# Performance work log

Hardware: AMD Instinct MI355X
Metric: run time of the kernel (lower is better)

The kernel has to match this reference:

```python
import jax, jax.numpy as jnp
import numpy as np

LAMBDA_CHAMFER = 1.0
LAMBDA_EDGE = 0.1


def setup_inputs() -> dict:
    key = jax.random.key(0)
    k1, k2, k3 = jax.random.split(key, 3)
    B, N, M, E = 8, 4096, 4096, 12288
    pred_vertices = jax.random.normal(k1, (B, N, 3), dtype=jnp.float32)
    gt_vertices = jax.random.normal(k2, (B, M, 3), dtype=jnp.float32)
    edges = jax.random.randint(k3, (E, 2), 0, N, dtype=jnp.int64)
    return {"pred_vertices": pred_vertices, "gt_vertices": gt_vertices, "edges": edges}


def _pairwise_dist(p1, p2):
    # ||x - y|| computed via the expanded form to avoid a [B,N,M,3] intermediate.
    # dist2[b,n,m] = |p1[b,n]|^2 + |p2[b,m]|^2 - 2 * p1[b,n] . p2[b,m]
    sq1 = jnp.sum(p1 * p1, axis=-1)  # [B, N]
    sq2 = jnp.sum(p2 * p2, axis=-1)  # [B, M]
    cross = jnp.einsum('bnd,bmd->bnm', p1, p2)  # [B, N, M]
    dist2 = sq1[:, :, None] + sq2[:, None, :] - 2.0 * cross
    return jnp.sqrt(jnp.maximum(dist2, 0.0))


def chamfer_distance(p1, p2):
    dist = _pairwise_dist(p1, p2)  # [B, N, M]
    min_p1 = jnp.min(dist, axis=2)  # [B, N] nearest gt for each pred point
    min_p2 = jnp.min(dist, axis=1)  # [B, M] nearest pred for each gt point
    return jnp.mean(min_p1) + jnp.mean(min_p2)


def edge_length_regularization(vertices, edges):
    v1 = vertices[:, edges[:, 0]]  # [B, E, 3]
    v2 = vertices[:, edges[:, 1]]  # [B, E, 3]
    lengths = jnp.linalg.norm(v1 - v2, axis=2)  # [B, E]
    return jnp.var(lengths, ddof=1)  # torch.var is unbiased by default


def reference(pred_vertices, gt_vertices, edges):
    cd = chamfer_distance(pred_vertices, gt_vertices)
    edge_loss = edge_length_regularization(pred_vertices, edges)
    return LAMBDA_CHAMFER * cd + LAMBDA_EDGE * edge_loss
```

## Files before the change

kernel.cpp:

```cpp
#include <hip/hip_runtime.h>
#include <hip/hip_bf16.h>
#include <float.h>

constexpr int B = 8, N = 4096, M = 4096, E = 12288;
constexpr int CBLOCK = 1024;
constexpr int CHAM_BLOCKS = 256;
constexpr int EDGE_BLOCKS = (B * E) / CBLOCK;
constexpr int SPLIT = 8;
constexpr int RPT = M / SPLIT;
constexpr int VEC = 2;
constexpr int QG = CBLOCK / SPLIT;


__global__ __launch_bounds__(CBLOCK) void fused_kernel(
    const float* __restrict__ pred, const float* __restrict__ gt,
    const int* __restrict__ edges, float* __restrict__ ws) {
    const int bid = blockIdx.x;
    const int t = threadIdx.x;

    __shared__ float4 tile[M];
    __shared__ float red[SPLIT * 256];
    __shared__ float wsum[16];

    if (bid < CHAM_BLOCKS) {
        const int dir = bid >> 7;
        const int b   = (bid >> 4) & 7;
        const int qt  = bid & 15;
        const float* __restrict__ q   = dir ? gt   : pred;
        const float* __restrict__ ref = dir ? pred : gt;

        {
            const float2* rb = (const float2*)(ref + (size_t)b * M * 3) + 6 * t;
            const float2 r0 = rb[0], r1 = rb[1], r2 = rb[2];
            const float2 r3 = rb[3], r4 = rb[4], r5 = rb[5];
            const float x0=r0.x,y0=r0.y,z0=r1.x, x1=r1.y,y1=r2.x,z1=r2.y;
            const float x2=r3.x,y2=r3.y,z2=r4.x, x3=r4.y,y3=r5.x,z3=r5.y;
            tile[4*t+0] = make_float4(x0,y0,z0, 0.5f*(x0*x0+y0*y0+z0*z0));
            tile[4*t+1] = make_float4(x1,y1,z1, 0.5f*(x1*x1+y1*y1+z1*z1));
            tile[4*t+2] = make_float4(x2,y2,z2, 0.5f*(x2*x2+y2*y2+z2*z2));
            tile[4*t+3] = make_float4(x3,y3,z3, 0.5f*(x3*x3+y3*y3+z3*z3));
        }

        const int qloc = t & (QG - 1);
        const int s    = t >> 7;
        float qx[VEC], qy[VEC], qz[VEC], h1[VEC];
#pragma unroll
        for (int i = 0; i < VEC; i++) {
            const int n = qt * 256 + qloc + i * QG;
            const float* qp = q + ((size_t)b * N + n) * 3;
            qx[i] = qp[0]; qy[i] = qp[1]; qz[i] = qp[2];
            h1[i] = 0.5f * (qx[i]*qx[i] + qy[i]*qy[i] + qz[i]*qz[i]);
        }
        __syncthreads();

        const float4* tl = tile + s * RPT;
        float mnA[VEC], mnB[VEC];
#pragma unroll
        for (int i = 0; i < VEC; i++) { mnA[i] = FLT_MAX; mnB[i] = FLT_MAX; }

#pragma unroll 2
        for (int m = 0; m < RPT; m += 4) {
            const float4 p0 = tl[m], p1 = tl[m+1], p2 = tl[m+2], p3 = tl[m+3];
#pragma unroll
            for (int i = 0; i < VEC; i++) {
                float d0 = h1[i] + p0.w;
                d0 = fmaf(-qx[i], p0.x, d0); d0 = fmaf(-qy[i], p0.y, d0); d0 = fmaf(-qz[i], p0.z, d0);
                float d1 = h1[i] + p1.w;
                d1 = fmaf(-qx[i], p1.x, d1); d1 = fmaf(-qy[i], p1.y, d1); d1 = fmaf(-qz[i], p1.z, d1);
                float d2 = h1[i] + p2.w;
                d2 = fmaf(-qx[i], p2.x, d2); d2 = fmaf(-qy[i], p2.y, d2); d2 = fmaf(-qz[i], p2.z, d2);
                float d3 = h1[i] + p3.w;
                d3 = fmaf(-qx[i], p3.x, d3); d3 = fmaf(-qy[i], p3.y, d3); d3 = fmaf(-qz[i], p3.z, d3);
                mnA[i] = fminf(mnA[i], fminf(d0, d1));
                mnB[i] = fminf(mnB[i], fminf(d2, d3));
            }
        }

        red[s * 256 + qloc]      = fminf(mnA[0], mnB[0]);
        red[s * 256 + qloc + QG] = fminf(mnA[1], mnB[1]);
        __syncthreads();

        float sv = 0.0f;
        if (t < 256) {
            float m8 = red[t];
#pragma unroll
            for (int k = 1; k < SPLIT; k++) m8 = fminf(m8, red[k * 256 + t]);
            sv = sqrtf(fmaxf(2.0f * m8, 0.0f));
        }
#pragma unroll
        for (int o = 32; o > 0; o >>= 1) sv += __shfl_down(sv, o, 64);
        if ((t & 63) == 0) wsum[t >> 6] = sv;
        __syncthreads();
        if (t == 0) ws[bid] = wsum[0] + wsum[1] + wsum[2] + wsum[3];
    } else {
        const int eg = (bid - CHAM_BLOCKS) * CBLOCK + t;
        const int b  = eg / E;
        const int e  = eg - b * E;
        const int i0 = edges[2 * e], i1 = edges[2 * e + 1];
        const float* p0 = pred + ((size_t)b * N + i0) * 3;
        const float* p1 = pred + ((size_t)b * N + i1) * 3;
        const float dx = p0[0] - p1[0];
        const float dy = p0[1] - p1[1];
        const float dz = p0[2] - p1[2];
        float L  = sqrtf(dx * dx + dy * dy + dz * dz);
        float L2 = L * L;
#pragma unroll
        for (int o = 32; o > 0; o >>= 1) {
            L  += __shfl_down(L, o, 64);
            L2 += __shfl_down(L2, o, 64);
        }
        if ((t & 63) == 0) { red[t >> 6] = L; red[32 + (t >> 6)] = L2; }
        __syncthreads();
        if (t == 0) {
            float a = 0.0f, c = 0.0f;
#pragma unroll
            for (int w = 0; w < 16; w++) { a += red[w]; c += red[32 + w]; }
            const int eb = bid - CHAM_BLOCKS;
            ws[CHAM_BLOCKS + 2 * eb]     = a;
            ws[CHAM_BLOCKS + 2 * eb + 1] = c;
        }
    }
}

__global__ __launch_bounds__(256) void final_kernel(
    const float* __restrict__ ws, float* __restrict__ out) {
    const int t = threadIdx.x;
    float sc = ws[t];
    float s1 = 0.0f, s2 = 0.0f;
    if (t < EDGE_BLOCKS) {
        s1 = ws[CHAM_BLOCKS + 2 * t];
        s2 = ws[CHAM_BLOCKS + 2 * t + 1];
    }
#pragma unroll
    for (int o = 32; o > 0; o >>= 1) {
        sc += __shfl_down(sc, o, 64);
        s1 += __shfl_down(s1, o, 64);
        s2 += __shfl_down(s2, o, 64);
    }
    __shared__ float w[3][4];
    const int wv = t >> 6, ln = t & 63;
    if (ln == 0) { w[0][wv] = sc; w[1][wv] = s1; w[2][wv] = s2; }
    __syncthreads();
    if (t == 0) {
        float S = 0.0f, A = 0.0f, C = 0.0f;
#pragma unroll
        for (int i = 0; i < 4; i++) { S += w[0][i]; A += w[1][i]; C += w[2][i]; }
        const float K = (float)(B * E);
        const float var = (C - A * A / K) / (K - 1.0f);
        out[0] = S / 32768.0f + 0.1f * var;
    }
}

extern "C" void kernel_launch(void* const* d_in, const int* in_sizes, int n_in,
                              void* d_out, int out_size, void* d_ws, size_t ws_size,
                              hipStream_t stream) {
    const float* pred  = (const float*)d_in[0];
    const float* gt    = (const float*)d_in[1];
    const int*   edges = (const int*)d_in[2];
    float* out = (float*)d_out;
    float* wsf = (float*)d_ws;

    fused_kernel<<<CHAM_BLOCKS + EDGE_BLOCKS, CBLOCK, 0, stream>>>(pred, gt, edges, wsf);
    final_kernel<<<1, 256, 0, stream>>>(wsf, out);
}
```

Before: 87.29 us.

## Raise per-thread query count, split ref across 32 slices, reorder edge blocks first

```diff
diff --git a/kernel.cpp b/kernel.cpp
--- a/kernel.cpp
+++ b/kernel.cpp
@@ -4,12 +4,12 @@
 
 constexpr int B = 8, N = 4096, M = 4096, E = 12288;
 constexpr int CBLOCK = 1024;
-constexpr int CHAM_BLOCKS = 256;
 constexpr int EDGE_BLOCKS = (B * E) / CBLOCK;
-constexpr int SPLIT = 8;
+constexpr int CHAM_BLOCKS = 2 * B * (N / 256);
+constexpr int SPLIT = 32;
 constexpr int RPT = M / SPLIT;
-constexpr int VEC = 2;
-constexpr int QG = CBLOCK / SPLIT;
+constexpr int VEC = 8;
+constexpr int QB = 256;
 
 
 __global__ __launch_bounds__(CBLOCK) void fused_kernel(
@@ -19,13 +19,14 @@
     const int t = threadIdx.x;
 
     __shared__ float4 tile[M];
-    __shared__ float red[SPLIT * 256];
     __shared__ float wsum[16];
+    float* red = (float*)tile;
 
-    if (bid < CHAM_BLOCKS) {
-        const int dir = bid >> 7;
-        const int b   = (bid >> 4) & 7;
-        const int qt  = bid & 15;
+    if (bid >= EDGE_BLOCKS) {
+        const int cb  = bid - EDGE_BLOCKS;
+        const int dir = cb >> 7;
+        const int b   = (cb >> 4) & 7;
+        const int qt  = cb & 15;
         const float* __restrict__ q   = dir ? gt   : pred;
         const float* __restrict__ ref = dir ? pred : gt;
 
@@ -41,12 +42,12 @@
             tile[4*t+3] = make_float4(x3,y3,z3, 0.5f*(x3*x3+y3*y3+z3*z3));
         }
 
-        const int qloc = t & (QG - 1);
-        const int s    = t >> 7;
+        const int qloc = t & 31;
+        const int s    = t >> 5;
         float qx[VEC], qy[VEC], qz[VEC], h1[VEC];
 #pragma unroll
         for (int i = 0; i < VEC; i++) {
-            const int n = qt * 256 + qloc + i * QG;
+            const int n = qt * QB + qloc + i * 32;
             const float* qp = q + ((size_t)b * N + n) * 3;
             qx[i] = qp[0]; qy[i] = qp[1]; qz[i] = qp[2];
             h1[i] = 0.5f * (qx[i]*qx[i] + qy[i]*qy[i] + qz[i]*qz[i]);
@@ -54,46 +55,64 @@
         __syncthreads();
 
         const float4* tl = tile + s * RPT;
-        float mnA[VEC], mnB[VEC];
+        float mn[VEC];
 #pragma unroll
-        for (int i = 0; i < VEC; i++) { mnA[i] = FLT_MAX; mnB[i] = FLT_MAX; }
+        for (int i = 0; i < VEC; i++) mn[i] = FLT_MAX;
 
+        float4 pA = tl[0], pB = tl[1];
 #pragma unroll 2
-        for (int m = 0; m < RPT; m += 4) {
-            const float4 p0 = tl[m], p1 = tl[m+1], p2 = tl[m+2], p3 = tl[m+3];
+        for (int m = 0; m < RPT - 2; m += 2) {
+            const float4 nA = tl[m + 2], nB = tl[m + 3];
 #pragma unroll
             for (int i = 0; i < VEC; i++) {
-                float d0 = h1[i] + p0.w;
-                d0 = fmaf(-qx[i], p0.x, d0); d0 = fmaf(-qy[i], p0.y, d0); d0 = fmaf(-qz[i], p0.z, d0);
-                float d1 = h1[i] + p1.w;
-                d1 = fmaf(-qx[i], p1.x, d1); d1 = fmaf(-qy[i], p1.y, d1); d1 = fmaf(-qz[i], p1.z, d1);
-                float d2 = h1[i] + p2.w;
-                d2 = fmaf(-qx[i], p2.x, d2); d2 = fmaf(-qy[i], p2.y, d2); d2 = fmaf(-qz[i], p2.z, d2);
-                float d3 = h1[i] + p3.w;
-                d3 = fmaf(-qx[i], p3.x, d3); d3 = fmaf(-qy[i], p3.y, d3); d3 = fmaf(-qz[i], p3.z, d3);
-                mnA[i] = fminf(mnA[i], fminf(d0, d1));
-                mnB[i] = fminf(mnB[i], fminf(d2, d3));
+                float d0 = fmaf(-qx[i], pA.x, h1[i] + pA.w);
+                d0 = fmaf(-qy[i], pA.y, d0);
+                d0 = fmaf(-qz[i], pA.z, d0);
+                float d1 = fmaf(-qx[i], pB.x, h1[i] + pB.w);
+                d1 = fmaf(-qy[i], pB.y, d1);
+                d1 = fmaf(-qz[i], pB.z, d1);
+                mn[i] = fminf(mn[i], fminf(d0, d1));
             }
+            pA = nA; pB = nB;
         }
+#pragma unroll
+        for (int i = 0; i < VEC; i++) {
+            float d0 = fmaf(-qx[i], pA.x, h1[i] + pA.w);
+            d0 = fmaf(-qy[i], pA.y, d0);
+            d0 = fmaf(-qz[i], pA.z, d0);
+            float d1 = fmaf(-qx[i], pB.x, h1[i] + pB.w);
+            d1 = fmaf(-qy[i], pB.y, d1);
+            d1 = fmaf(-qz[i], pB.z, d1);
+            mn[i] = fminf(mn[i], fminf(d0, d1));
+        }
+        __syncthreads();
 
-        red[s * 256 + qloc]      = fminf(mnA[0], mnB[0]);
-        red[s * 256 + qloc + QG] = fminf(mnA[1], mnB[1]);
+        const int wv = t >> 6;
+#pragma unroll
+        for (int i = 0; i < VEC; i++)
+            mn[i] = fminf(mn[i], __shfl_xor(mn[i], 32, 64));
+        if ((t & 32) == 0) {
+#pragma unroll
+            for (int i = 0; i < VEC; i++)
+                red[(qloc + i * 32) + 256 * wv] = mn[i];
+        }
         __syncthreads();
 
         float sv = 0.0f;
-        if (t < 256) {
-            float m8 = red[t];
+        if (t < QB) {
+            float m = red[t];
 #pragma unroll
-            for (int k = 1; k < SPLIT; k++) m8 = fminf(m8, red[k * 256 + t]);
-            sv = sqrtf(fmaxf(2.0f * m8, 0.0f));
+            for (int w = 1; w < 16; w++) m = fminf(m, red[t + 256 * w]);
+            sv = sqrtf(fmaxf(2.0f * m, 0.0f));
         }
 #pragma unroll
         for (int o = 32; o > 0; o >>= 1) sv += __shfl_down(sv, o, 64);
-        if ((t & 63) == 0) wsum[t >> 6] = sv;
+        if ((t & 63) == 0) wsum[wv] = sv;
         __syncthreads();
-        if (t == 0) ws[bid] = wsum[0] + wsum[1] + wsum[2] + wsum[3];
+        if (t == 0)
+            ws[2 * EDGE_BLOCKS + cb] = wsum[0] + wsum[1] + wsum[2] + wsum[3];
     } else {
-        const int eg = (bid - CHAM_BLOCKS) * CBLOCK + t;
+        const int eg = bid * CBLOCK + t;
         const int b  = eg / E;
         const int e  = eg - b * E;
         const int i0 = edges[2 * e], i1 = edges[2 * e + 1];
@@ -115,9 +134,8 @@
             float a = 0.0f, c = 0.0f;
 #pragma unroll
             for (int w = 0; w < 16; w++) { a += red[w]; c += red[32 + w]; }
-            const int eb = bid - CHAM_BLOCKS;
-            ws[CHAM_BLOCKS + 2 * eb]     = a;
-            ws[CHAM_BLOCKS + 2 * eb + 1] = c;
+            ws[2 * bid]     = a;
+            ws[2 * bid + 1] = c;
         }
     }
 }
@@ -125,11 +143,11 @@
 __global__ __launch_bounds__(256) void final_kernel(
     const float* __restrict__ ws, float* __restrict__ out) {
     const int t = threadIdx.x;
-    float sc = ws[t];
+    float sc = ws[2 * EDGE_BLOCKS + t];
     float s1 = 0.0f, s2 = 0.0f;
     if (t < EDGE_BLOCKS) {
-        s1 = ws[CHAM_BLOCKS + 2 * t];
-        s2 = ws[CHAM_BLOCKS + 2 * t + 1];
+        s1 = ws[2 * t];
+        s2 = ws[2 * t + 1];
     }
 #pragma unroll
     for (int o = 32; o > 0; o >>= 1) {
@@ -160,6 +178,6 @@
     float* out = (float*)d_out;
     float* wsf = (float*)d_ws;
 
-    fused_kernel<<<CHAM_BLOCKS + EDGE_BLOCKS, CBLOCK, 0, stream>>>(pred, gt, edges, wsf);
+    fused_kernel<<<EDGE_BLOCKS + CHAM_BLOCKS, CBLOCK, 0, stream>>>(pred, gt, edges, wsf);
     final_kernel<<<1, 256, 0, stream>>>(wsf, out);
 }
```

After: 85.04 us. 2.6% less time.
